# Kernel optimization log

Hardware: AMD Instinct MI355X
Metric: run time of the kernel (lower is better)

Reference implementation:

```python
import jax, jax.numpy as jnp
import numpy as np
from jax import lax

T, P, EPS = 8, 3, 1e-5


def setup_inputs() -> dict:
    key = jax.random.key(0)
    ks = jax.random.split(key, 12)
    n, c, h, w = 16, 512, 28, 28
    r = c // 8
    sc = 1.0 / np.sqrt(c).astype(np.float32)
    return {
        "X": jax.random.normal(ks[0], (n * T, c, h, w), jnp.float32),
        "conv1_w": jax.random.normal(ks[1], (r, c, 1, 1, 1), jnp.float32) * 0.05,
        "conv1_b": jnp.zeros((r,), jnp.float32),
        "g1": jnp.ones((r,), jnp.float32),
        "b1": jnp.zeros((r,), jnp.float32),
        "m1": jax.random.normal(ks[2], (r,), jnp.float32) * 0.1,
        "v1": jax.random.uniform(ks[3], (r,), jnp.float32, 0.5, 1.5),
        "conv2_w": jax.random.normal(ks[4], (r, r, 3, 1, 1), jnp.float32) * 0.05,
        "conv2_b": jnp.zeros((r,), jnp.float32),
        "conv3_w": jax.random.normal(ks[5], (P, r, 1, 5, 5), jnp.float32) * 0.05,
        "conv3_b": jnp.zeros((P,), jnp.float32),
        "g2": jnp.ones((P,), jnp.float32),
        "b2": jnp.zeros((P,), jnp.float32),
        "m2": jax.random.normal(ks[6], (P,), jnp.float32) * 0.1,
        "v2": jax.random.uniform(ks[7], (P,), jnp.float32, 0.5, 1.5),
        "gcn0_w": jax.random.normal(ks[8], (c, c), jnp.float32) * sc,
        "gcn1_w": jax.random.normal(ks[9], (c, c), jnp.float32) * sc,
        "att_w": jax.random.normal(ks[10], (1, c), jnp.float32) * sc,
        "att_b": jnp.zeros((1,), jnp.float32),
    }


def _conv3d(x, w, b, pad):
    y = lax.conv_general_dilated(x, w, (1, 1, 1), pad,
                                 dimension_numbers=("NCDHW", "OIDHW", "NCDHW"))
    return y + b[None, :, None, None, None]


def _bn(x, g, b, m, v):
    # eval-mode BatchNorm3d folded into scale/shift
    inv = g * lax.rsqrt(v + EPS)
    return x * inv[None, :, None, None, None] + (b - m * inv)[None, :, None, None, None]


def _lrelu(x):
    return jnp.where(x >= 0, x, 0.05 * x)


def reference(X, conv1_w, conv1_b, g1, b1, m1, v1, conv2_w, conv2_b,
              conv3_w, conv3_b, g2, b2, m2, v2, gcn0_w, gcn1_w, att_w, att_b):
    nt, c, h, w = X.shape
    n = nt // T
    Xr = X.reshape(n, T, c, h, w)
    residual = Xr.mean((3, 4))                          # [n,t,c]
    Xp = jnp.transpose(Xr, (0, 2, 1, 3, 4))             # [n,c,t,h,w]

    # saliency detector
    s = _lrelu(_bn(_conv3d(Xp, conv1_w, conv1_b, [(0, 0)] * 3), g1, b1, m1, v1))
    s = _conv3d(s, conv2_w, conv2_b, [(1, 1), (0, 0), (0, 0)])
    s = _conv3d(s, conv3_w, conv3_b, [(0, 0), (2, 2), (2, 2)])
    s_map = jax.nn.sigmoid(_bn(s, g2, b2, m2, v2))      # [n,P,t,h,w]

    # weighted node pooling (avoids the [n,c,P,t,h,w] broadcast intermediate)
    nodes = jnp.einsum('ncthw,npthw->ntpc', Xp, s_map) / (h * w)
    nodes = nodes.reshape(n, T * P, c)                  # [n,N,c], N=24

    # normalized Laplacian as elementwise outer-product scaling
    A = jnp.einsum('nic,njc->nij', nodes, nodes) / c
    deg = jnp.clip(A.sum(-1), 1e-8, None)
    dinv = deg ** -0.5
    L = dinv[:, :, None] * A * dinv[:, None, :]

    # GCN (2 bias-free layers) + attention readout
    Xg = nodes
    for W in (gcn0_w, gcn1_w):
        Xg = _lrelu(L @ (Xg @ W.T))
    att = jax.nn.softmax(L @ ((Xg + nodes) @ att_w.T) + att_b, axis=1)  # [n,N,1]
    readout = (Xg * att).sum(1)                         # [n,c]
    return jnp.concatenate([readout[:, None, :], residual], axis=1)  # [n,t+1,c]
```

## Files before the change

### kernel.cpp

```cpp
#include <hip/hip_runtime.h>
#include <hip/hip_bf16.h>
#include <math.h>

#define NT 128
#define NB 16
#define TT 8
#define C 512
#define RR 64
#define HW 784
#define HH 28
#define WW 28
#define PP 3
#define NN 24
#define EPS 1e-5f

typedef __attribute__((ext_vector_type(8))) short bh8;
typedef __attribute__((ext_vector_type(4))) float f32x4;
typedef unsigned short u16;
typedef unsigned int u32;

static __device__ inline u16 f2bf(float f) {
    __hip_bfloat16 h = __float2bfloat16(f);
    return *(u16*)&h;
}
static __device__ inline float bf2f(u16 u) {
    __hip_bfloat16 h;
    *(u16*)&h = u;
    return __bfloat162float(h);
}
static __device__ inline void pack8(const float* x, u32* hp, u32* lp) {
    #pragma unroll
    for (int i = 0; i < 4; ++i) {
        u16 h0 = f2bf(x[2 * i]), h1 = f2bf(x[2 * i + 1]);
        u16 l0 = f2bf(x[2 * i] - bf2f(h0));
        u16 l1 = f2bf(x[2 * i + 1] - bf2f(h1));
        hp[i] = (u32)h0 | ((u32)h1 << 16);
        lp[i] = (u32)l0 | ((u32)l1 << 16);
    }
}

__global__ __launch_bounds__(256) void convA_mfma(const float* __restrict__ X,
        const float* __restrict__ W1, const float* __restrict__ cb,
        const float* __restrict__ g, const float* __restrict__ bb,
        const float* __restrict__ m, const float* __restrict__ v,
        u32* __restrict__ s1p)
{
    __shared__ u16 Xh[128 * 32];
    __shared__ u16 Xl[128 * 32];
    __shared__ u16 Wh[4 * 64 * 8];
    __shared__ u16 Wl[4 * 64 * 8];
    __shared__ float sInv[64], sAdd[64], sCb[64];

    const int nt  = blockIdx.y;
    const int hw0 = blockIdx.x * 128;
    const int tid = threadIdx.x;

    if (tid < 64) {
        float inv = g[tid] * rsqrtf(v[tid] + EPS);
        sInv[tid] = inv;
        sAdd[tid] = bb[tid] - m[tid] * inv;
        sCb[tid]  = cb[tid];
    }

    const int hwl = tid & 127;
    const int kg  = tid >> 7;
    const int hw_g = hw0 + hwl;
    const bool hok = hw_g < HW;
    const int wr = tid >> 2, wj = tid & 3;
    const int w  = tid >> 6, l = tid & 63;
    const int rh = w >> 1, hh = w & 1;
    const int gq = l >> 4, mm = l & 15;
    const int rslot = gq ^ (mm & 3) ^ ((mm >> 2) & 3);

    f32x4 acc[2][4];
    #pragma unroll
    for (int i = 0; i < 2; ++i)
        #pragma unroll
        for (int jj = 0; jj < 4; ++jj) acc[i][jj] = (f32x4){0.f, 0.f, 0.f, 0.f};

    const float* Xnt = X + (size_t)nt * C * HW;

    for (int k0 = 0; k0 < C; k0 += 32) {
        float xv[16];
        #pragma unroll
        for (int j = 0; j < 16; ++j)
            xv[j] = hok ? Xnt[(size_t)(k0 + kg * 16 + j) * HW + hw_g] : 0.f;
        const float* wsrc = W1 + (size_t)wr * C + k0 + wj * 8;
        float4 wa = *(const float4*)wsrc;
        float4 wb = *(const float4*)(wsrc + 4);

        __syncthreads();
        #pragma unroll
        for (int q = 0; q < 2; ++q) {
            u32 hp[4], lp[4];
            pack8(&xv[q * 8], hp, lp);
            int slot = ((kg << 1) | q) ^ (hwl & 3) ^ ((hwl >> 2) & 3);
            *(uint4*)&Xh[hwl * 32 + slot * 8] = make_uint4(hp[0], hp[1], hp[2], hp[3]);
            *(uint4*)&Xl[hwl * 32 + slot * 8] = make_uint4(lp[0], lp[1], lp[2], lp[3]);
        }
        {
            float x[8] = {wa.x, wa.y, wa.z, wa.w, wb.x, wb.y, wb.z, wb.w};
            u32 hp[4], lp[4];
            pack8(x, hp, lp);
            int woff = ((wr >> 4) * 64 + (wr & 15) + 16 * wj) * 8;
            *(uint4*)&Wh[woff] = make_uint4(hp[0], hp[1], hp[2], hp[3]);
            *(uint4*)&Wl[woff] = make_uint4(lp[0], lp[1], lp[2], lp[3]);
        }
        __syncthreads();

        bh8 fxh[4], fxl[4];
        #pragma unroll
        for (int nb = 0; nb < 4; ++nb) {
            int hwrow = (hh << 6) + (nb << 4) + mm;
            fxh[nb] = *(const bh8*)&Xh[hwrow * 32 + rslot * 8];
            fxl[nb] = *(const bh8*)&Xl[hwrow * 32 + rslot * 8];
        }
        #pragma unroll
        for (int rr = 0; rr < 2; ++rr) {
            int rt = (rh << 1) | rr;
            bh8 wh = *(const bh8*)&Wh[(rt * 64 + l) * 8];
            bh8 wl = *(const bh8*)&Wl[(rt * 64 + l) * 8];
            #pragma unroll
            for (int nb = 0; nb < 4; ++nb) {
                acc[rr][nb] = __builtin_amdgcn_mfma_f32_16x16x32_bf16(wh, fxh[nb], acc[rr][nb], 0, 0, 0);
                acc[rr][nb] = __builtin_amdgcn_mfma_f32_16x16x32_bf16(wh, fxl[nb], acc[rr][nb], 0, 0, 0);
                acc[rr][nb] = __builtin_amdgcn_mfma_f32_16x16x32_bf16(wl, fxh[nb], acc[rr][nb], 0, 0, 0);
            }
        }
    }

    #pragma unroll
    for (int rr = 0; rr < 2; ++rr) {
        #pragma unroll
        for (int nb = 0; nb < 4; ++nb) {
            int hw = hw0 + (hh << 6) + (nb << 4) + mm;
            if (hw < HW) {
                #pragma unroll
                for (int reg = 0; reg < 4; ++reg) {
                    int r = (((rh << 1) | rr) << 4) + (gq << 2) + reg;
                    float y = (acc[rr][nb][reg] + sCb[r]) * sInv[r] + sAdd[r];
                    y = (y >= 0.f) ? y : 0.05f * y;
                    u16 h = f2bf(y);
                    u16 lo = f2bf(y - bf2f(h));
                    s1p[((size_t)nt * RR + r) * HW + hw] = (u32)h | ((u32)lo << 16);
                }
            }
        }
    }
}

__global__ __launch_bounds__(256) void convB_mfma(const u32* __restrict__ s1p,
        const float* __restrict__ W2, const float* __restrict__ cb,
        float* __restrict__ s2)
{
    __shared__ u16 Xh[128 * 32];
    __shared__ u16 Xl[128 * 32];
    __shared__ u16 Wh[2 * 2048];
    __shared__ u16 Wl[2 * 2048];

    const int nt  = blockIdx.y;
    const int n = nt >> 3, t = nt & 7;
    const int hw0 = blockIdx.x * 128;
    const int tid = threadIdx.x;

    const int hwl = tid & 127;
    const int kg  = tid >> 7;
    const int hw_g = hw0 + hwl;
    const bool hok = hw_g < HW;
    const int wr = tid >> 2, wj = tid & 3;
    const int w  = tid >> 6, l = tid & 63;
    const int rh = w >> 1, hh = w & 1;
    const int gq = l >> 4, mm = l & 15;
    const int rslot = gq ^ (mm & 3) ^ ((mm >> 2) & 3);

    f32x4 acc[2][4];
    #pragma unroll
    for (int i = 0; i < 2; ++i)
        #pragma unroll
        for (int jj = 0; jj < 4; ++jj) acc[i][jj] = (f32x4){0.f, 0.f, 0.f, 0.f};

    for (int dt = 0; dt < 3; ++dt) {
        int tp = t + dt - 1;
        if (tp < 0 || tp >= TT) continue;
        __syncthreads();
        #pragma unroll
        for (int kc = 0; kc < 2; ++kc) {
            const float* wsrc = W2 + (size_t)wr * 192 + (kc * 32 + wj * 8) * 3 + dt;
            float x[8];
            #pragma unroll
            for (int i = 0; i < 8; ++i) x[i] = wsrc[i * 3];
            u32 hp[4], lp[4];
            pack8(x, hp, lp);
            int woff = kc * 2048 + ((wr >> 4) * 64 + (wr & 15) + 16 * wj) * 8;
            *(uint4*)&Wh[woff] = make_uint4(hp[0], hp[1], hp[2], hp[3]);
            *(uint4*)&Wl[woff] = make_uint4(lp[0], lp[1], lp[2], lp[3]);
        }
        const size_t pbase = (size_t)(n * TT + tp) * RR * HW;
        #pragma unroll
        for (int kc = 0; kc < 2; ++kc) {
            u32 xv[16];
            #pragma unroll
            for (int j = 0; j < 16; ++j)
                xv[j] = hok ? s1p[pbase + (size_t)(kc * 32 + kg * 16 + j) * HW + hw_g] : 0u;
            __syncthreads();
            #pragma unroll
            for (int q = 0; q < 2; ++q) {
                u32 hp[4], lp[4];
                #pragma unroll
                for (int i = 0; i < 4; ++i) {
                    u32 u0 = xv[q * 8 + 2 * i], u1 = xv[q * 8 + 2 * i + 1];
                    hp[i] = (u0 & 0xffffu) | (u1 << 16);
                    lp[i] = (u0 >> 16) | (u1 & 0xffff0000u);
                }
                int slot = ((kg << 1) | q) ^ (hwl & 3) ^ ((hwl >> 2) & 3);
                *(uint4*)&Xh[hwl * 32 + slot * 8] = make_uint4(hp[0], hp[1], hp[2], hp[3]);
                *(uint4*)&Xl[hwl * 32 + slot * 8] = make_uint4(lp[0], lp[1], lp[2], lp[3]);
            }
            __syncthreads();

            bh8 fxh[4], fxl[4];
            #pragma unroll
            for (int nb = 0; nb < 4; ++nb) {
                int hwrow = (hh << 6) + (nb << 4) + mm;
                fxh[nb] = *(const bh8*)&Xh[hwrow * 32 + rslot * 8];
                fxl[nb] = *(const bh8*)&Xl[hwrow * 32 + rslot * 8];
            }
            #pragma unroll
            for (int rr = 0; rr < 2; ++rr) {
                int rt = (rh << 1) | rr;
                bh8 wh = *(const bh8*)&Wh[kc * 2048 + (rt * 64 + l) * 8];
                bh8 wl = *(const bh8*)&Wl[kc * 2048 + (rt * 64 + l) * 8];
                #pragma unroll
                for (int nb = 0; nb < 4; ++nb) {
                    acc[rr][nb] = __builtin_amdgcn_mfma_f32_16x16x32_bf16(wh, fxh[nb], acc[rr][nb], 0, 0, 0);
                    acc[rr][nb] = __builtin_amdgcn_mfma_f32_16x16x32_bf16(wh, fxl[nb], acc[rr][nb], 0, 0, 0);
                    acc[rr][nb] = __builtin_amdgcn_mfma_f32_16x16x32_bf16(wl, fxh[nb], acc[rr][nb], 0, 0, 0);
                }
            }
        }
    }

    #pragma unroll
    for (int rr = 0; rr < 2; ++rr) {
        #pragma unroll
        for (int nb = 0; nb < 4; ++nb) {
            int hw = hw0 + (hh << 6) + (nb << 4) + mm;
            if (hw < HW) {
                #pragma unroll
                for (int reg = 0; reg < 4; ++reg) {
                    int r = (((rh << 1) | rr) << 4) + (gq << 2) + reg;
                    s2[((size_t)nt * RR + r) * HW + hw] = acc[rr][nb][reg] + cb[r];
                }
            }
        }
    }
}

__global__ __launch_bounds__(256) void convC_sw(const float* __restrict__ s2,
        const float* __restrict__ W3, float* __restrict__ partial)
{
    const int tid  = threadIdx.x;
    const int wave = tid >> 6;
    const int lane = tid & 63;
    const int half = lane >> 5;
    const int col  = lane & 31;
    const int item = blockIdx.x * 8 + wave * 2 + half;
    const int band = item & 3;
    const int nt   = (item >> 2) & 127;
    int cg = item >> 9;
    cg = __builtin_amdgcn_readfirstlane(cg);

    const int row0 = band * 7;
    const bool cok = (col < 28);

    float acc[3][7];
    #pragma unroll
    for (int p = 0; p < 3; ++p)
        #pragma unroll
        for (int r = 0; r < 7; ++r) acc[p][r] = 0.f;

    for (int chi = 0; chi < 8; ++chi) {
        float wgt[75];
        #pragma unroll
        for (int p = 0; p < 3; ++p)
            #pragma unroll
            for (int q = 0; q < 25; ++q)
                wgt[p * 25 + q] = W3[(size_t)(p * 64 + cg * 8 + chi) * 25 + q];

        const float* src = s2 + ((size_t)nt * RR + cg * 8 + chi) * HW;
        float wdw[5][5];

        #pragma unroll
        for (int rr = 0; rr < 4; ++rr) {
            int R = row0 - 2 + rr;
            bool rok = (R >= 0) & (R < HH);
            #pragma unroll
            for (int j = 0; j < 5; ++j) {
                int cc = col - 2 + j;
                bool ok = rok & cok & (cc >= 0) & (cc < WW);
                wdw[rr][j] = ok ? src[R * WW + cc] : 0.f;
            }
        }
        #pragma unroll
        for (int r = 0; r < 7; ++r) {
            {
                int R = row0 + 2 + r;
                bool rok = (R < HH);
                int slot = (r + 4) % 5;
                #pragma unroll
                for (int j = 0; j < 5; ++j) {
                    int cc = col - 2 + j;
                    bool ok = rok & cok & (cc >= 0) & (cc < WW);
                    wdw[slot][j] = ok ? src[R * WW + cc] : 0.f;
                }
            }
            #pragma unroll
            for (int p = 0; p < 3; ++p)
                #pragma unroll
                for (int dh = 0; dh < 5; ++dh)
                    #pragma unroll
                    for (int dw = 0; dw < 5; ++dw)
                        acc[p][r] += wdw[(r + dh) % 5][dw] * wgt[p * 25 + dh * 5 + dw];
        }
    }

    if (cok) {
        #pragma unroll
        for (int p = 0; p < 3; ++p)
            #pragma unroll
            for (int r = 0; r < 7; ++r)
                partial[(((size_t)cg * 128 + nt) * 3 + p) * HW + (row0 + r) * WW + col]
                    = acc[p][r];
    }
}

__global__ __launch_bounds__(256) void convC_fin(const float* __restrict__ partial,
        const float* __restrict__ cb, const float* __restrict__ g,
        const float* __restrict__ bb, const float* __restrict__ m,
        const float* __restrict__ v, float* __restrict__ smap)
{
    const int idx = blockIdx.x * 256 + threadIdx.x;
    const int total = 128 * 3 * HW;
    if (idx >= total) return;
    const int p = (idx / HW) % 3;
    float a = cb[p];
    #pragma unroll
    for (int gg = 0; gg < 8; ++gg) a += partial[(size_t)gg * total + idx];
    float inv = g[p] * rsqrtf(v[p] + EPS);
    float z = a * inv + (bb[p] - m[p] * inv);
    smap[idx] = 1.f / (1.f + expf(-z));
}

__global__ __launch_bounds__(256) void poolD(const float* __restrict__ X,
        const float* __restrict__ smap, float* __restrict__ nodes,
        float* __restrict__ out)
{
    const int tid = threadIdx.x;
    const int lane = tid & 63;
    const int gw = blockIdx.x * 4 + (tid >> 6);
    const int c = gw & 511;
    const int nt = gw >> 9;
    const float4* X4 = (const float4*)(X + ((size_t)nt * C + c) * HW);
    const float4* S0 = (const float4*)(smap + (size_t)nt * PP * HW);
    const float4* S1 = S0 + 196;
    const float4* S2 = S1 + 196;
    float sx = 0.f, a0 = 0.f, a1 = 0.f, a2 = 0.f;
    #pragma unroll
    for (int i = 0; i < 4; ++i) {
        int fi = i * 64 + lane;
        if (fi < 196) {
            float4 x = X4[fi];
            float4 p0 = S0[fi], p1 = S1[fi], p2 = S2[fi];
            sx += x.x + x.y + x.z + x.w;
            a0 += x.x * p0.x + x.y * p0.y + x.z * p0.z + x.w * p0.w;
            a1 += x.x * p1.x + x.y * p1.y + x.z * p1.z + x.w * p1.w;
            a2 += x.x * p2.x + x.y * p2.y + x.z * p2.z + x.w * p2.w;
        }
    }
    #pragma unroll
    for (int off = 32; off >= 1; off >>= 1) {
        sx += __shfl_xor(sx, off);
        a0 += __shfl_xor(a0, off);
        a1 += __shfl_xor(a1, off);
        a2 += __shfl_xor(a2, off);
    }
    if (lane == 0) {
        int n = nt >> 3, t = nt & 7;
        const float s = 1.f / 784.f;
        out[((size_t)n * 9 + 1 + t) * C + c] = sx * s;
        float* nd = nodes + ((size_t)n * NN + t * PP) * C + c;
        nd[0]     = a0 * s;
        nd[C]     = a1 * s;
        nd[2 * C] = a2 * s;
    }
}

__global__ __launch_bounds__(256) void graphL(const float* __restrict__ nodes,
        float* __restrict__ Lg)
{
    __shared__ float4 nds[24][129];
    __shared__ float Amat[24][24];
    __shared__ float dinv[24];
    const int n = blockIdx.x;
    const int tid = threadIdx.x;
    const float4* src = (const float4*)(nodes + (size_t)n * NN * C);
    #pragma unroll
    for (int i = 0; i < 12; ++i) {
        int fi = tid + i * 256;
        int row = fi >> 7, k4 = fi & 127;
        nds[row][k4] = src[row * 128 + k4];
    }
    __syncthreads();
    for (int pair = tid; pair < 576; pair += 256) {
        int i = pair / 24, j = pair - (pair / 24) * 24;
        const float4* ri = &nds[i][0];
        const float4* rj = &nds[j][0];
        float s = 0.f;
        for (int k = 0; k < 128; ++k) {
            float4 a = ri[k], b = rj[k];
            s += a.x * b.x + a.y * b.y + a.z * b.z + a.w * b.w;
        }
        Amat[i][j] = s * (1.f / 512.f);
    }
    __syncthreads();
    if (tid < 24) {
        float d = 0.f;
        for (int j = 0; j < 24; ++j) d += Amat[tid][j];
        d = fmaxf(d, 1e-8f);
        dinv[tid] = 1.f / sqrtf(d);
    }
    __syncthreads();
    for (int pair = tid; pair < 576; pair += 256) {
        int i = pair / 24, j = pair - (pair / 24) * 24;
        Lg[(size_t)n * 576 + pair] = dinv[i] * Amat[i][j] * dinv[j];
    }
}

__global__ __launch_bounds__(256) void gemmG(const float* __restrict__ Xin,
        const float* __restrict__ Wm, float* __restrict__ Y)
{
    __shared__ float Xs[32][36];
    __shared__ float Ws[32][66];
    const int o0 = blockIdx.x * 64;
    const int m0 = blockIdx.y * 32;
    const int tid = threadIdx.x;
    const int tr = tid >> 5;
    const int tc = tid & 31;
    float acc[4][2] = {};

    for (int k0 = 0; k0 < 512; k0 += 32) {
        {
            int ml = tid >> 3, k4 = tid & 7;
            float4 xv = *(const float4*)&Xin[(size_t)(m0 + ml) * 512 + k0 + k4 * 4];
            Xs[k4 * 4 + 0][ml] = xv.x; Xs[k4 * 4 + 1][ml] = xv.y;
            Xs[k4 * 4 + 2][ml] = xv.z; Xs[k4 * 4 + 3][ml] = xv.w;
        }
        #pragma unroll
        for (int i = 0; i < 2; ++i) {
            int idx = tid + i * 256;
            int ol = idx >> 3, k4 = idx & 7;
            float4 wv = *(const float4*)&Wm[(size_t)(o0 + ol) * 512 + k0 + k4 * 4];
            Ws[k4 * 4 + 0][ol] = wv.x; Ws[k4 * 4 + 1][ol] = wv.y;
            Ws[k4 * 4 + 2][ol] = wv.z; Ws[k4 * 4 + 3][ol] = wv.w;
        }
        __syncthreads();
        #pragma unroll
        for (int k = 0; k < 32; ++k) {
            float4 xv = *(const float4*)&Xs[k][tr * 4];
            float2 wv = *(const float2*)&Ws[k][tc * 2];
            acc[0][0] += xv.x * wv.x; acc[0][1] += xv.x * wv.y;
            acc[1][0] += xv.y * wv.x; acc[1][1] += xv.y * wv.y;
            acc[2][0] += xv.z * wv.x; acc[2][1] += xv.z * wv.y;
            acc[3][0] += xv.w * wv.x; acc[3][1] += xv.w * wv.y;
        }
        __syncthreads();
    }
    #pragma unroll
    for (int i2 = 0; i2 < 4; ++i2)
        #pragma unroll
        for (int j = 0; j < 2; ++j)
            Y[(size_t)(m0 + tr * 4 + i2) * 512 + o0 + tc * 2 + j] = acc[i2][j];
}

__global__ __launch_bounds__(256) void applyL(const float* __restrict__ G,
        const float* __restrict__ Lg, float* __restrict__ Xg)
{
    __shared__ float Ls[576];
    const int n = blockIdx.y;
    const int tid = threadIdx.x;
    for (int i = tid; i < 576; i += 256) Ls[i] = Lg[(size_t)n * 576 + i];
    __syncthreads();
    const int o = blockIdx.x * 128 + (tid & 127);
    const int ig = (tid >> 7) * 12;
    float acc[12] = {};
    const float* Gn = G + (size_t)n * NN * 512;
    for (int j = 0; j < 24; ++j) {
        float gv = Gn[j * 512 + o];
        #pragma unroll
        for (int i = 0; i < 12; ++i)
            acc[i] += Ls[(ig + i) * 24 + j] * gv;
    }
    float* Xn = Xg + (size_t)n * NN * 512;
    #pragma unroll
    for (int i = 0; i < 12; ++i) {
        float y = acc[i];
        Xn[(ig + i) * 512 + o] = (y >= 0.f) ? y : 0.05f * y;
    }
}

__global__ __launch_bounds__(256) void attE(const float* __restrict__ Xg,
        const float* __restrict__ nodes, const float* __restrict__ Lg,
        const float* __restrict__ aw, const float* __restrict__ ab,
        float* __restrict__ out)
{
    __shared__ float zs[24], ys[24], att[24], Ls[576];
    const int n = blockIdx.x;
    const int tid = threadIdx.x;
    const int lane = tid & 63, wv = tid >> 6;
    for (int i = tid; i < 576; i += 256) Ls[i] = Lg[(size_t)n * 576 + i];
    const float* Xn = Xg + (size_t)n * NN * 512;
    const float* Nn = nodes + (size_t)n * NN * 512;
    for (int i = wv; i < 24; i += 4) {
        float s = 0.f;
        #pragma unroll
        for (int kk = 0; kk < 8; ++kk) {
            int k = kk * 64 + lane;
            s += (Xn[i * 512 + k] + Nn[i * 512 + k]) * aw[k];
        }
        #pragma unroll
        for (int off = 32; off >= 1; off >>= 1) s += __shfl_xor(s, off);
        if (lane == 0) zs[i] = s;
    }
    __syncthreads();
    if (tid < 24) {
        float y = ab[0];
        for (int j = 0; j < 24; ++j) y += Ls[tid * 24 + j] * zs[j];
        ys[tid] = y;
    }
    __syncthreads();
    if (tid < 64) {
        float vv = (tid < 24) ? ys[tid] : -3.4e38f;
        float mx = vv;
        #pragma unroll
        for (int off = 32; off >= 1; off >>= 1) mx = fmaxf(mx, __shfl_xor(mx, off));
        float e = (tid < 24) ? expf(vv - mx) : 0.f;
        float ssum = e;
        #pragma unroll
        for (int off = 32; off >= 1; off >>= 1) ssum += __shfl_xor(ssum, off);
        if (tid < 24) att[tid] = e / ssum;
    }
    __syncthreads();
    for (int c2 = tid; c2 < 512; c2 += 256) {
        float r = 0.f;
        #pragma unroll
        for (int i = 0; i < 24; ++i) r += Xn[i * 512 + c2] * att[i];
        out[(size_t)n * 9 * 512 + c2] = r;
    }
}

extern "C" void kernel_launch(void* const* d_in, const int* in_sizes, int n_in,
                              void* d_out, int out_size, void* d_ws, size_t ws_size,
                              hipStream_t stream)
{
    const float* X   = (const float*)d_in[0];
    const float* w1  = (const float*)d_in[1];
    const float* b1c = (const float*)d_in[2];
    const float* g1  = (const float*)d_in[3];
    const float* b1  = (const float*)d_in[4];
    const float* m1  = (const float*)d_in[5];
    const float* v1  = (const float*)d_in[6];
    const float* w2  = (const float*)d_in[7];
    const float* b2c = (const float*)d_in[8];
    const float* w3  = (const float*)d_in[9];
    const float* b3c = (const float*)d_in[10];
    const float* g2  = (const float*)d_in[11];
    const float* b2  = (const float*)d_in[12];
    const float* m2  = (const float*)d_in[13];
    const float* v2  = (const float*)d_in[14];
    const float* gw0 = (const float*)d_in[15];
    const float* gw1 = (const float*)d_in[16];
    const float* aw  = (const float*)d_in[17];
    const float* ab  = (const float*)d_in[18];
    float* out = (float*)d_out;

    const size_t S1N = (size_t)NT * RR * HW;
    u32*   s1p   = (u32*)d_ws;
    float* part  = (float*)d_ws;
    float* s2    = (float*)(s1p + S1N);
    float* smap  = s2 + S1N;
    float* nodes = smap + (size_t)NT * PP * HW;
    float* Lg    = nodes + (size_t)NB * NN * C;
    float* gt    = Lg + (size_t)NB * NN * NN;
    float* xa    = gt + (size_t)NB * NN * C;
    float* xb    = xa + (size_t)NB * NN * C;

    convA_mfma<<<dim3(7, NT), 256, 0, stream>>>(X, w1, b1c, g1, b1, m1, v1, s1p);
    convB_mfma<<<dim3(7, NT), 256, 0, stream>>>(s1p, w2, b2c, s2);
    convC_sw<<<dim3(512), 256, 0, stream>>>(s2, w3, part);
    convC_fin<<<dim3(1176), 256, 0, stream>>>(part, b3c, g2, b2, m2, v2, smap);
    poolD<<<dim3(16384), 256, 0, stream>>>(X, smap, nodes, out);
    graphL<<<dim3(NB), 256, 0, stream>>>(nodes, Lg);
    gemmG<<<dim3(8, 12), 256, 0, stream>>>(nodes, gw0, gt);
    applyL<<<dim3(4, NB), 256, 0, stream>>>(gt, Lg, xa);
    gemmG<<<dim3(8, 12), 256, 0, stream>>>(xa, gw1, gt);
    applyL<<<dim3(4, NB), 256, 0, stream>>>(gt, Lg, xb);
    attE<<<dim3(NB), 256, 0, stream>>>(xb, nodes, Lg, aw, ab, out);
}
```

Measured before the change: 503.3 us.

## Prefetch next K-slice in conv GEMMs and stage saliency map in LDS for pooling

```diff
diff --git a/kernel.cpp b/kernel.cpp
--- a/kernel.cpp
+++ b/kernel.cpp
@@ -80,15 +80,18 @@
 
     const float* Xnt = X + (size_t)nt * C * HW;
 
+    float xv[16];
+    float4 wa, wb;
+    #pragma unroll
+    for (int j = 0; j < 16; ++j)
+        xv[j] = hok ? Xnt[(size_t)(kg * 16 + j) * HW + hw_g] : 0.f;
+    {
+        const float* wsrc = W1 + (size_t)wr * C + wj * 8;
+        wa = *(const float4*)wsrc;
+        wb = *(const float4*)(wsrc + 4);
+    }
+
     for (int k0 = 0; k0 < C; k0 += 32) {
-        float xv[16];
-        #pragma unroll
-        for (int j = 0; j < 16; ++j)
-            xv[j] = hok ? Xnt[(size_t)(k0 + kg * 16 + j) * HW + hw_g] : 0.f;
-        const float* wsrc = W1 + (size_t)wr * C + k0 + wj * 8;
-        float4 wa = *(const float4*)wsrc;
-        float4 wb = *(const float4*)(wsrc + 4);
-
         __syncthreads();
         #pragma unroll
         for (int q = 0; q < 2; ++q) {
@@ -107,6 +110,15 @@
             *(uint4*)&Wl[woff] = make_uint4(lp[0], lp[1], lp[2], lp[3]);
         }
         __syncthreads();
+
+        if (k0 + 32 < C) {
+            #pragma unroll
+            for (int j = 0; j < 16; ++j)
+                xv[j] = hok ? Xnt[(size_t)(k0 + 32 + kg * 16 + j) * HW + hw_g] : 0.f;
+            const float* wsrc = W1 + (size_t)wr * C + k0 + 32 + wj * 8;
+            wa = *(const float4*)wsrc;
+            wb = *(const float4*)(wsrc + 4);
+        }
 
         bh8 fxh[4], fxl[4];
         #pragma unroll
@@ -173,35 +185,34 @@
     const int gq = l >> 4, mm = l & 15;
     const int rslot = gq ^ (mm & 3) ^ ((mm >> 2) & 3);
 
+    const int dtlo = (t == 0) ? 1 : 0;
+    const int dthi = (t == 7) ? 1 : 2;
+
     f32x4 acc[2][4];
     #pragma unroll
     for (int i = 0; i < 2; ++i)
         #pragma unroll
         for (int jj = 0; jj < 4; ++jj) acc[i][jj] = (f32x4){0.f, 0.f, 0.f, 0.f};
 
-    for (int dt = 0; dt < 3; ++dt) {
-        int tp = t + dt - 1;
-        if (tp < 0 || tp >= TT) continue;
-        __syncthreads();
+    u32 xv[16];
+    float wx[2][8];
+
+    {
+        int tp = t + dtlo - 1;
+        size_t pbase = (size_t)(n * TT + tp) * RR * HW;
+        #pragma unroll
+        for (int j = 0; j < 16; ++j)
+            xv[j] = hok ? s1p[pbase + (size_t)(kg * 16 + j) * HW + hw_g] : 0u;
+        #pragma unroll
+        for (int kc2 = 0; kc2 < 2; ++kc2)
+            #pragma unroll
+            for (int i = 0; i < 8; ++i)
+                wx[kc2][i] = W2[(size_t)wr * 192 + (kc2 * 32 + wj * 8 + i) * 3 + dtlo];
+    }
+
+    for (int dt = dtlo; dt <= dthi; ++dt) {
         #pragma unroll
         for (int kc = 0; kc < 2; ++kc) {
-            const float* wsrc = W2 + (size_t)wr * 192 + (kc * 32 + wj * 8) * 3 + dt;
-            float x[8];
-            #pragma unroll
-            for (int i = 0; i < 8; ++i) x[i] = wsrc[i * 3];
-            u32 hp[4], lp[4];
-            pack8(x, hp, lp);
-            int woff = kc * 2048 + ((wr >> 4) * 64 + (wr & 15) + 16 * wj) * 8;
-            *(uint4*)&Wh[woff] = make_uint4(hp[0], hp[1], hp[2], hp[3]);
-            *(uint4*)&Wl[woff] = make_uint4(lp[0], lp[1], lp[2], lp[3]);
-        }
-        const size_t pbase = (size_t)(n * TT + tp) * RR * HW;
-        #pragma unroll
-        for (int kc = 0; kc < 2; ++kc) {
-            u32 xv[16];
-            #pragma unroll
-            for (int j = 0; j < 16; ++j)
-                xv[j] = hok ? s1p[pbase + (size_t)(kc * 32 + kg * 16 + j) * HW + hw_g] : 0u;
             __syncthreads();
             #pragma unroll
             for (int q = 0; q < 2; ++q) {
@@ -216,7 +227,36 @@
                 *(uint4*)&Xh[hwl * 32 + slot * 8] = make_uint4(hp[0], hp[1], hp[2], hp[3]);
                 *(uint4*)&Xl[hwl * 32 + slot * 8] = make_uint4(lp[0], lp[1], lp[2], lp[3]);
             }
+            if (kc == 0) {
+                #pragma unroll
+                for (int kc2 = 0; kc2 < 2; ++kc2) {
+                    u32 hp[4], lp[4];
+                    pack8(wx[kc2], hp, lp);
+                    int woff = kc2 * 2048 + ((wr >> 4) * 64 + (wr & 15) + 16 * wj) * 8;
+                    *(uint4*)&Wh[woff] = make_uint4(hp[0], hp[1], hp[2], hp[3]);
+                    *(uint4*)&Wl[woff] = make_uint4(lp[0], lp[1], lp[2], lp[3]);
+                }
+            }
             __syncthreads();
+
+            if (kc == 0) {
+                int tp = t + dt - 1;
+                size_t pbase = (size_t)(n * TT + tp) * RR * HW;
+                #pragma unroll
+                for (int j = 0; j < 16; ++j)
+                    xv[j] = hok ? s1p[pbase + (size_t)(32 + kg * 16 + j) * HW + hw_g] : 0u;
+            } else if (dt < dthi) {
+                int tp = t + dt;
+                size_t pbase = (size_t)(n * TT + tp) * RR * HW;
+                #pragma unroll
+                for (int j = 0; j < 16; ++j)
+                    xv[j] = hok ? s1p[pbase + (size_t)(kg * 16 + j) * HW + hw_g] : 0u;
+                #pragma unroll
+                for (int kc2 = 0; kc2 < 2; ++kc2)
+                    #pragma unroll
+                    for (int i = 0; i < 8; ++i)
+                        wx[kc2][i] = W2[(size_t)wr * 192 + (kc2 * 32 + wj * 8 + i) * 3 + dt + 1];
+            }
 
             bh8 fxh[4], fxl[4];
             #pragma unroll
@@ -355,43 +395,50 @@
         const float* __restrict__ smap, float* __restrict__ nodes,
         float* __restrict__ out)
 {
+    __shared__ float sm[3 * HW];
     const int tid = threadIdx.x;
-    const int lane = tid & 63;
-    const int gw = blockIdx.x * 4 + (tid >> 6);
-    const int c = gw & 511;
-    const int nt = gw >> 9;
-    const float4* X4 = (const float4*)(X + ((size_t)nt * C + c) * HW);
-    const float4* S0 = (const float4*)(smap + (size_t)nt * PP * HW);
-    const float4* S1 = S0 + 196;
-    const float4* S2 = S1 + 196;
-    float sx = 0.f, a0 = 0.f, a1 = 0.f, a2 = 0.f;
-    #pragma unroll
-    for (int i = 0; i < 4; ++i) {
-        int fi = i * 64 + lane;
-        if (fi < 196) {
-            float4 x = X4[fi];
-            float4 p0 = S0[fi], p1 = S1[fi], p2 = S2[fi];
-            sx += x.x + x.y + x.z + x.w;
-            a0 += x.x * p0.x + x.y * p0.y + x.z * p0.z + x.w * p0.w;
-            a1 += x.x * p1.x + x.y * p1.y + x.z * p1.z + x.w * p1.w;
-            a2 += x.x * p2.x + x.y * p2.y + x.z * p2.z + x.w * p2.w;
-        }
-    }
-    #pragma unroll
-    for (int off = 32; off >= 1; off >>= 1) {
-        sx += __shfl_xor(sx, off);
-        a0 += __shfl_xor(a0, off);
-        a1 += __shfl_xor(a1, off);
-        a2 += __shfl_xor(a2, off);
-    }
-    if (lane == 0) {
-        int n = nt >> 3, t = nt & 7;
-        const float s = 1.f / 784.f;
-        out[((size_t)n * 9 + 1 + t) * C + c] = sx * s;
-        float* nd = nodes + ((size_t)n * NN + t * PP) * C + c;
-        nd[0]     = a0 * s;
-        nd[C]     = a1 * s;
-        nd[2 * C] = a2 * s;
+    const int nt = blockIdx.x >> 2;
+    const int q  = blockIdx.x & 3;
+    const float* S = smap + (size_t)nt * PP * HW;
+    for (int idx = tid; idx < 3 * HW; idx += 256) sm[idx] = S[idx];
+    __syncthreads();
+
+    const int wv = tid >> 6, lane = tid & 63;
+    const int n = nt >> 3, t = nt & 7;
+    const float s = 1.f / 784.f;
+
+    for (int ci = 0; ci < 32; ++ci) {
+        const int c = q * 128 + wv * 32 + ci;
+        const float4* X4 = (const float4*)(X + ((size_t)nt * C + c) * HW);
+        float sx = 0.f, a0 = 0.f, a1 = 0.f, a2 = 0.f;
+        #pragma unroll
+        for (int i = 0; i < 4; ++i) {
+            int fi = i * 64 + lane;
+            if (fi < 196) {
+                float4 x = X4[fi];
+                float4 p0 = *(const float4*)&sm[0 * HW + fi * 4];
+                float4 p1 = *(const float4*)&sm[1 * HW + fi * 4];
+                float4 p2 = *(const float4*)&sm[2 * HW + fi * 4];
+                sx += x.x + x.y + x.z + x.w;
+                a0 += x.x * p0.x + x.y * p0.y + x.z * p0.z + x.w * p0.w;
+                a1 += x.x * p1.x + x.y * p1.y + x.z * p1.z + x.w * p1.w;
+                a2 += x.x * p2.x + x.y * p2.y + x.z * p2.z + x.w * p2.w;
+            }
+        }
+        #pragma unroll
+        for (int off = 32; off >= 1; off >>= 1) {
+            sx += __shfl_xor(sx, off);
+            a0 += __shfl_xor(a0, off);
+            a1 += __shfl_xor(a1, off);
+            a2 += __shfl_xor(a2, off);
+        }
+        if (lane == 0) {
+            out[((size_t)n * 9 + 1 + t) * C + c] = sx * s;
+            float* nd = nodes + ((size_t)n * NN + t * PP) * C + c;
+            nd[0]     = a0 * s;
+            nd[C]     = a1 * s;
+            nd[2 * C] = a2 * s;
+        }
     }
 }
 
@@ -598,7 +645,7 @@
     convB_mfma<<<dim3(7, NT), 256, 0, stream>>>(s1p, w2, b2c, s2);
     convC_sw<<<dim3(512), 256, 0, stream>>>(s2, w3, part);
     convC_fin<<<dim3(1176), 256, 0, stream>>>(part, b3c, g2, b2, m2, v2, smap);
-    poolD<<<dim3(16384), 256, 0, stream>>>(X, smap, nodes, out);
+    poolD<<<dim3(512), 256, 0, stream>>>(X, smap, nodes, out);
     graphL<<<dim3(NB), 256, 0, stream>>>(nodes, Lg);
     gemmG<<<dim3(8, 12), 256, 0, stream>>>(nodes, gw0, gt);
     applyL<<<dim3(4, NB), 256, 0, stream>>>(gt, Lg, xa);
```

After: 509.2 us. No clear change (+1.2%).
